# Kernel optimization log

Measured on AMD Instinct MI355X. Metric: run time of the kernel, lower is better.

## Reference

```python
import jax, jax.numpy as jnp
import numpy as np

NPOINT = 2048
NSAMPLE = 32
BN_EPS = 1e-5


def fps(xyz_t, npoint):
    """Furthest point sampling. xyz_t: [B,N,3] -> idx [B,npoint] (starts at index 0)."""
    B, N, _ = xyz_t.shape

    def step(carry, _):
        dist, last = carry  # dist [B,N], last [B]
        centroid = jnp.take_along_axis(xyz_t, last[:, None, None], axis=1)  # [B,1,3]
        d = jnp.sum((xyz_t - centroid) ** 2, axis=-1)  # [B,N]
        dist = jnp.minimum(dist, d)
        nxt = jnp.argmax(dist, axis=1).astype(jnp.int32)
        return (dist, nxt), last

    init = (jnp.full((B, N), 1e10, xyz_t.dtype), jnp.zeros((B,), jnp.int32))
    _, idx = jax.lax.scan(step, init, None, length=npoint)  # [npoint,B]
    return jnp.transpose(idx)  # [B,npoint]


def knn(k, query_t, ref_t):
    """query_t [B,S,3], ref_t [B,N,3] -> k-nearest indices [B,S,k]."""
    d = (jnp.sum(query_t ** 2, -1)[:, :, None]
         + jnp.sum(ref_t ** 2, -1)[:, None, :]
         - 2.0 * jnp.einsum('bsc,bnc->bsn', query_t, ref_t))  # [B,S,N]
    _, idx = jax.lax.top_k(-d, k)
    return idx


def group(feat_t, idx):
    """feat_t [B,N,C], idx [B,S,K] -> [B,S,K,C] gathered neighbors."""
    return jax.vmap(lambda f, i: f[i])(feat_t, idx)


def setup_inputs():
    key = jax.random.key(0)
    ks = jax.random.split(key, 8)
    B, N, C, D = 8, 8192, 3, 3
    mlp = [32, 32, 64]
    inp = {
        'xyz': jax.random.normal(ks[0], (B, C, N), jnp.float32),
        'points': jax.random.normal(ks[1], (B, D, N), jnp.float32),
    }
    last = D + 3  # conv input channels = in_channel + 3
    for i, oc in enumerate(mlp):
        inp[f'w{i}'] = jax.random.normal(ks[2 + i], (oc, last), jnp.float32) * (1.0 / np.sqrt(last))
        inp[f'g{i}'] = jnp.ones((oc,), jnp.float32)
        inp[f'b{i}'] = jnp.zeros((oc,), jnp.float32)
        last = oc
    return inp


def reference(xyz, points, w0, g0, b0, w1, g1, b1, w2, g2, b2):
    xyz_t = jnp.transpose(xyz, (0, 2, 1))        # [B,N,3]
    points_t = jnp.transpose(points, (0, 2, 1))  # [B,N,D]

    fps_idx = fps(xyz_t, NPOINT)                             # [B,S]
    new_xyz_t = jax.vmap(lambda f, i: f[i])(xyz_t, fps_idx)  # [B,S,3]

    knn_idx = knn(NSAMPLE, new_xyz_t, xyz_t)                 # [B,S,K]
    grouped_xyz = group(xyz_t, knn_idx)                      # [B,S,K,3]
    pos_diff = grouped_xyz - new_xyz_t[:, :, None, :]        # [B,S,K,3]
    grouped_pts = group(points_t, knn_idx)                   # [B,S,K,D]

    x = jnp.concatenate([pos_diff, grouped_pts], axis=-1)    # [B,S,K,3+D]
    for w, g, b in ((w0, g0, b0), (w1, g1, b1), (w2, g2, b2)):
        x = jnp.einsum('oc,bskc->bsko', w, x)                # 1x1 conv, no bias
        mean = jnp.mean(x, axis=(0, 1, 2))                   # BatchNorm2d (training stats)
        var = jnp.var(x, axis=(0, 1, 2))
        x = jax.nn.relu(g * (x - mean) * jax.lax.rsqrt(var + BN_EPS) + b)

    new_points = jnp.max(x, axis=2)  # max over K neighbors -> [B,S,C']
    new_xyz = jnp.transpose(new_xyz_t, (0, 2, 1))      # [B,3,S]
    new_points = jnp.transpose(new_points, (0, 2, 1))  # [B,C',S]
    return (new_xyz, new_points, fps_idx)
```

## Files before the change

kernel.cpp:

```cpp
#include <hip/hip_runtime.h>
#include <hip/hip_bf16.h>
#include <math.h>


#define NB 8
#define NN 8192
#define NS 2048
#define NK 32

typedef float f32x2 __attribute__((ext_vector_type(2)));

__device__ __forceinline__ f32x2 pk_mul(f32x2 a, f32x2 b) {
  f32x2 d; asm("v_pk_mul_f32 %0, %1, %2" : "=v"(d) : "v"(a), "v"(b)); return d;
}
__device__ __forceinline__ f32x2 pk_add(f32x2 a, f32x2 b) {
  f32x2 d; asm("v_pk_add_f32 %0, %1, %2" : "=v"(d) : "v"(a), "v"(b)); return d;
}
__device__ __forceinline__ f32x2 pk_sub(f32x2 a, f32x2 b) {
  f32x2 d;
  asm("v_pk_add_f32 %0, %1, %2 neg_lo:[0,1] neg_hi:[0,1]" : "=v"(d) : "v"(a), "v"(b));
  return d;
}

__global__ __launch_bounds__(256) void prep_kernel(const float* __restrict__ xyz,
                                                   const float* __restrict__ pts,
                                                   float4* __restrict__ xyz4,
                                                   float4* __restrict__ pts4) {
  int g = blockIdx.x * 256 + threadIdx.x;
  int b = g >> 13, n = g & 8191;
  const float* xb = xyz + b * 3 * NN;
  float x = xb[n], y = xb[NN + n], z = xb[2 * NN + n];
  xyz4[g] = make_float4(x, y, z, fmaf(x, x, fmaf(y, y, z * z)));
  const float* pb = pts + b * 3 * NN;
  pts4[g] = make_float4(pb[n], pb[NN + n], pb[2 * NN + n], 0.f);
}

template <int CTRL>
__device__ __forceinline__ float dpp_max(float v) {
  int o = __builtin_amdgcn_update_dpp(__float_as_int(v), __float_as_int(v),
                                      CTRL, 0xf, 0xf, false);
  return fmaxf(v, __int_as_float(o));
}

__global__ __launch_bounds__(512, 1) void fps_kernel(const float4* __restrict__ xyz4,
                                                     float* __restrict__ out_nxyz,
                                                     float* __restrict__ out_fps,
                                                     float4* __restrict__ nxyz4) {
#pragma clang fp contract(off)
  int b = blockIdx.x, tid = threadIdx.x;
  int lane = tid & 63, wid = tid >> 6;
  __shared__ float4 tbl[NN];
  __shared__ unsigned long long kslot[2][8];
  const float4* xb = xyz4 + b * NN;

  f32x2 px[8], py[8], pz[8], dist[8];
#pragma unroll
  for (int jj = 0; jj < 8; ++jj) {
    float4 t0 = xb[(tid << 4) + 2 * jj];
    float4 t1 = xb[(tid << 4) + 2 * jj + 1];
    tbl[(tid << 4) + 2 * jj] = t0;
    tbl[(tid << 4) + 2 * jj + 1] = t1;
    px[jj] = (f32x2){t0.x, t1.x};
    py[jj] = (f32x2){t0.y, t1.y};
    pz[jj] = (f32x2){t0.z, t1.z};
    dist[jj] = (f32x2){1e10f, 1e10f};
  }

  float4 c0 = xb[0];
  float cx = c0.x, cy = c0.y, cz = c0.z;
  float* onx = out_nxyz + b * 3 * NS;
  if (tid == 0) {
    nxyz4[b * NS] = c0;
    onx[0] = c0.x;
    onx[NS] = c0.y;
    onx[2 * NS] = c0.z;
    out_fps[b * NS] = 0.f;
  }

  for (int s = 1; s < NS; ++s) {
    f32x2 c2x = {cx, cx}, c2y = {cy, cy}, c2z = {cz, cz};
#pragma unroll
    for (int jj = 0; jj < 8; ++jj) {
      f32x2 dx = pk_sub(px[jj], c2x);
      f32x2 dy = pk_sub(py[jj], c2y);
      f32x2 dz = pk_sub(pz[jj], c2z);
      f32x2 dd = pk_add(pk_add(pk_mul(dx, dx), pk_mul(dy, dy)), pk_mul(dz, dz));
      dist[jj] = __builtin_elementwise_min(dist[jj], dd);
    }
    f32x2 m2 = dist[0];
#pragma unroll
    for (int jj = 1; jj < 8; ++jj) m2 = __builtin_elementwise_max(m2, dist[jj]);
    float best = fmaxf(m2[0], m2[1]);
    int bj = 0;
#pragma unroll
    for (int j = 15; j >= 0; --j)
      bj = (dist[j >> 1][j & 1] == best) ? j : bj;

    float mm = best;
    mm = dpp_max<0x111>(mm);
    mm = dpp_max<0x112>(mm);
    mm = dpp_max<0x114>(mm);
    mm = dpp_max<0x118>(mm);
    mm = dpp_max<0x142>(mm);
    mm = dpp_max<0x143>(mm);
    float wmax = __int_as_float(__builtin_amdgcn_readlane(__float_as_int(mm), 63));

    unsigned long long bl = __ballot(best == wmax);
    int l0 = __ffsll(bl) - 1;
    int gw = __builtin_amdgcn_readlane((tid << 4) + bj, l0);

    if (lane == 0)
      kslot[s & 1][wid] = (((unsigned long long)__float_as_uint(wmax)) << 32) |
                          (unsigned)(8191 - gw);
    __syncthreads();

    const ulonglong2* kv = (const ulonglong2*)kslot[s & 1];
    ulonglong2 q0 = kv[0], q1 = kv[1], q2 = kv[2], q3 = kv[3];
    unsigned long long a0 = q0.x > q0.y ? q0.x : q0.y;
    unsigned long long a1 = q1.x > q1.y ? q1.x : q1.y;
    unsigned long long a2 = q2.x > q2.y ? q2.x : q2.y;
    unsigned long long a3 = q3.x > q3.y ? q3.x : q3.y;
    unsigned long long b0 = a0 > a1 ? a0 : a1;
    unsigned long long b1 = a2 > a3 ? a2 : a3;
    unsigned long long km = b0 > b1 ? b0 : b1;
    int gid = 8191 - (int)((unsigned)km & 0x1FFFu);
    gid = __builtin_amdgcn_readfirstlane(gid);

    float4 c = tbl[gid];
    cx = c.x; cy = c.y; cz = c.z;
    if (tid == 0) {
      nxyz4[b * NS + s] = c;
      onx[s] = c.x;
      onx[NS + s] = c.y;
      onx[2 * NS + s] = c.z;
      out_fps[b * NS + s] = (float)gid;
    }
  }
}

__device__ __forceinline__ void insert32(float (&a)[32], float f) {
#pragma unroll
  for (int i = 31; i >= 1; --i) a[i] = fminf(a[i], fmaxf(a[i - 1], f));
  a[0] = fminf(a[0], f);
}

__global__ __launch_bounds__(256) void knn_kernel(const float4* __restrict__ xyz4,
                                                  const float4* __restrict__ nxyz4,
                                                  int* __restrict__ knn) {
  __shared__ float lbuf[256][33];
  int b = blockIdx.x >> 5, tile = blockIdx.x & 31;
  int tid = threadIdx.x;
  int q = tid & 63, chunk = tid >> 6;
  float4 Q = nxyz4[b * NS + tile * 64 + q];
  float qq = Q.w;
  float mx = -2.f * Q.x, my = -2.f * Q.y, mz = -2.f * Q.z;
  float arr[32];
#pragma unroll
  for (int i = 0; i < 32; ++i) arr[i] = __uint_as_float(0x7f7fffffu);

  const float4* refs = xyz4 + b * NN + chunk * 2048;
  int rbase = chunk * 2048;
  for (int r = 0; r < 2048; ++r) {
    float4 R = refs[r];
    float d = fmaf(R.x, mx, fmaf(R.y, my, fmaf(R.z, mz, R.w + qq)));
    d = fmaxf(d, 0.f);
    float f = __uint_as_float((__float_as_uint(d) & 0xFFFFE000u) | (unsigned)(rbase + r));
    if (f < arr[31]) insert32(arr, f);
  }
#pragma unroll
  for (int i = 0; i < 32; ++i) lbuf[tid][i] = arr[i];
  __syncthreads();
  if (tid < 64) {
    for (int c = 1; c < 4; ++c)
      for (int i = 0; i < 32; ++i) {
        float f = lbuf[c * 64 + tid][i];
        if (f < arr[31]) insert32(arr, f);
      }
    int base = (b * NS + tile * 64 + tid) * NK;
#pragma unroll
    for (int i = 0; i < 32; ++i) knn[base + i] = (int)(__float_as_uint(arr[i]) & 0x1FFFu);
  }
}

template <int STAGE>
__global__ __launch_bounds__(256) void mlp_kernel(
    const float4* __restrict__ xyz4, const float4* __restrict__ pts4,
    const float4* __restrict__ nxyz4, const int* __restrict__ knn,
    const float* __restrict__ w0, const float* __restrict__ w1,
    const float* __restrict__ w2, const float* __restrict__ ab,
    float* __restrict__ partials, float* __restrict__ out_np) {
  constexpr int C = (STAGE == 2) ? 64 : 32;
  constexpr int SM = (STAGE == 3) ? 8 * 64 * 32 : 512;
  __shared__ float smem[SM];
  int blk = blockIdx.x;
  int b = blk >> 6, s0 = (blk & 63) * 32;
  int tid = threadIdx.x, sl = tid & 31, ksec = tid >> 5;
  int lane = tid & 63, wid = tid >> 6;
  int s = s0 + sl;
  float4 Q = nxyz4[b * NS + s];
  const float4* xb = xyz4 + b * NN;
  const float4* pb = pts4 + b * NN;
  const int* kb = knn + (b * NS + s) * NK + ksec * 4;

  float acc1[(STAGE == 3) ? 64 : C];
  float acc2[(STAGE == 3) ? 1 : C];
  if constexpr (STAGE == 3) {
#pragma unroll
    for (int o = 0; o < 64; ++o) acc1[o] = -3.4e38f;
  } else {
#pragma unroll
    for (int o = 0; o < C; ++o) { acc1[o] = 0.f; acc2[o] = 0.f; }
  }

  for (int kk = 0; kk < 4; ++kk) {
    int nid = kb[kk];
    float4 R = xb[nid];
    float4 P = pb[nid];
    float x0[6] = {R.x - Q.x, R.y - Q.y, R.z - Q.z, P.x, P.y, P.z};
    float h[32];
#pragma unroll
    for (int o = 0; o < 32; ++o) {
      float a = w0[o * 6] * x0[0];
#pragma unroll
      for (int c = 1; c < 6; ++c) a = fmaf(w0[o * 6 + c], x0[c], a);
      h[o] = a;
    }
    if constexpr (STAGE == 0) {
#pragma unroll
      for (int o = 0; o < 32; ++o) { acc1[o] += h[o]; acc2[o] = fmaf(h[o], h[o], acc2[o]); }
    } else {
#pragma unroll
      for (int o = 0; o < 32; ++o) h[o] = fmaxf(fmaf(h[o], ab[o], ab[64 + o]), 0.f);
      float h1[32];
#pragma unroll
      for (int o = 0; o < 32; ++o) {
        float a = 0.f;
#pragma unroll
        for (int i = 0; i < 32; ++i) a = fmaf(w1[o * 32 + i], h[i], a);
        h1[o] = a;
      }
      if constexpr (STAGE == 1) {
#pragma unroll
        for (int o = 0; o < 32; ++o) { acc1[o] += h1[o]; acc2[o] = fmaf(h1[o], h1[o], acc2[o]); }
      } else {
#pragma unroll
        for (int o = 0; o < 32; ++o) h1[o] = fmaxf(fmaf(h1[o], ab[128 + o], ab[192 + o]), 0.f);
#pragma unroll
        for (int o = 0; o < 64; ++o) {
          float a = 0.f;
#pragma unroll
          for (int i = 0; i < 32; ++i) a = fmaf(w2[o * 32 + i], h1[i], a);
          if constexpr (STAGE == 2) {
            acc1[o] += a;
            acc2[o] = fmaf(a, a, acc2[o]);
          } else {
            acc1[o] = fmaxf(acc1[o], fmaxf(fmaf(a, ab[256 + o], ab[320 + o]), 0.f));
          }
        }
      }
    }
  }

  if constexpr (STAGE < 3) {
#pragma unroll
    for (int o = 0; o < C; ++o) {
      float v1 = acc1[o], v2 = acc2[o];
#pragma unroll
      for (int d = 1; d < 64; d <<= 1) { v1 += __shfl_xor(v1, d); v2 += __shfl_xor(v2, d); }
      acc1[o] = v1; acc2[o] = v2;
    }
    if (lane == 0) {
#pragma unroll
      for (int o = 0; o < C; ++o) {
        smem[wid * 2 * C + o] = acc1[o];
        smem[wid * 2 * C + C + o] = acc2[o];
      }
    }
    __syncthreads();
    if (tid < 2 * C) {
      float v = smem[tid] + smem[2 * C + tid] + smem[4 * C + tid] + smem[6 * C + tid];
      partials[blk * 128 + tid] = v;
    }
  } else {
#pragma unroll
    for (int o = 0; o < 64; ++o) smem[ksec * 2048 + o * 32 + sl] = acc1[o];
    __syncthreads();
#pragma unroll
    for (int i = 0; i < 8; ++i) {
      int e = i * 256 + tid;
      int ch = e >> 5, ss = e & 31;
      float v = smem[ch * 32 + ss];
#pragma unroll
      for (int ks = 1; ks < 8; ++ks) v = fmaxf(v, smem[ks * 2048 + ch * 32 + ss]);
      out_np[b * 64 * NS + ch * NS + s0 + ss] = v;
    }
  }
}

__global__ __launch_bounds__(256) void finalize_kernel(const float* __restrict__ partials,
                                                       const float* __restrict__ g,
                                                       const float* __restrict__ bt,
                                                       float* __restrict__ ab, int C) {
  __shared__ float sm[256];
  int tid = threadIdx.x;
  int ch = tid & 127, half = tid >> 7;
  float acc = 0.f;
  if (ch < 2 * C) {
    const float* p = partials + half * 256 * 128 + ch;
    for (int i = 0; i < 256; ++i) acc += p[i * 128];
  }
  sm[half * 128 + ch] = acc;
  __syncthreads();
  if (tid < C) {
    float s1 = sm[tid] + sm[128 + tid];
    float s2 = sm[C + tid] + sm[128 + C + tid];
    const float ninv = 1.0f / 524288.0f;
    float mean = s1 * ninv;
    float var = s2 * ninv - mean * mean;
    float inv = 1.0f / sqrtf(var + 1e-5f);
    float a = g[tid] * inv;
    ab[tid] = a;
    ab[64 + tid] = bt[tid] - mean * a;
  }
}

extern "C" void kernel_launch(void* const* d_in, const int* in_sizes, int n_in,
                              void* d_out, int out_size, void* d_ws, size_t ws_size,
                              hipStream_t stream) {
  const float* xyz = (const float*)d_in[0];
  const float* pts = (const float*)d_in[1];
  const float* w0 = (const float*)d_in[2];
  const float* g0 = (const float*)d_in[3];
  const float* b0 = (const float*)d_in[4];
  const float* w1 = (const float*)d_in[5];
  const float* g1 = (const float*)d_in[6];
  const float* b1 = (const float*)d_in[7];
  const float* w2 = (const float*)d_in[8];
  const float* g2 = (const float*)d_in[9];
  const float* b2 = (const float*)d_in[10];
  float* out = (float*)d_out;
  float* ws = (float*)d_ws;

  float4* xyz4 = (float4*)ws;
  float4* pts4 = (float4*)(ws + 262144);
  float4* nxyz4 = (float4*)(ws + 524288);
  int* knn = (int*)(ws + 589824);
  float* partials = ws + 1114112;
  float* ab = ws + 1310720;
  float* out_np = out + 49152;
  float* out_fps = out + 1097728;

  prep_kernel<<<256, 256, 0, stream>>>(xyz, pts, xyz4, pts4);
  fps_kernel<<<NB, 512, 0, stream>>>(xyz4, out, out_fps, nxyz4);
  knn_kernel<<<256, 256, 0, stream>>>(xyz4, nxyz4, knn);

  mlp_kernel<0><<<512, 256, 0, stream>>>(xyz4, pts4, nxyz4, knn, w0, w1, w2, ab, partials, nullptr);
  finalize_kernel<<<1, 256, 0, stream>>>(partials, g0, b0, ab, 32);
  mlp_kernel<1><<<512, 256, 0, stream>>>(xyz4, pts4, nxyz4, knn, w0, w1, w2, ab, partials + 65536, nullptr);
  finalize_kernel<<<1, 256, 0, stream>>>(partials + 65536, g1, b1, ab + 128, 32);
  mlp_kernel<2><<<512, 256, 0, stream>>>(xyz4, pts4, nxyz4, knn, w0, w1, w2, ab, partials + 131072, nullptr);
  finalize_kernel<<<1, 256, 0, stream>>>(partials + 131072, g2, b2, ab + 256, 64);
  mlp_kernel<3><<<512, 256, 0, stream>>>(xyz4, pts4, nxyz4, knn, w0, w1, w2, ab, nullptr, out_np);
}
```

Measured before the change: 3.097 ms.

## Halve FPS block to 256 threads with 32 scalar points per thread

The furthest-point-sampling kernel now runs 4 waves per batch instead of 8, each thread holding 32 points in scalar registers instead of 16 in packed-float pairs. The aim is a cheaper cross-wave reduction and barrier per step, with fewer slots to combine. The per-thread argmax now uses a tree max followed by a bitmask search for the winning index, run only in lanes that hold the wave maximum. In exchange each thread does twice the distance work, using scalar instead of packed arithmetic, and register pressure rises.

```diff
diff --git a/kernel.cpp b/kernel.cpp
--- a/kernel.cpp
+++ b/kernel.cpp
@@ -7,20 +7,6 @@
 #define NN 8192
 #define NS 2048
 #define NK 32
-
-typedef float f32x2 __attribute__((ext_vector_type(2)));
-
-__device__ __forceinline__ f32x2 pk_mul(f32x2 a, f32x2 b) {
-  f32x2 d; asm("v_pk_mul_f32 %0, %1, %2" : "=v"(d) : "v"(a), "v"(b)); return d;
-}
-__device__ __forceinline__ f32x2 pk_add(f32x2 a, f32x2 b) {
-  f32x2 d; asm("v_pk_add_f32 %0, %1, %2" : "=v"(d) : "v"(a), "v"(b)); return d;
-}
-__device__ __forceinline__ f32x2 pk_sub(f32x2 a, f32x2 b) {
-  f32x2 d;
-  asm("v_pk_add_f32 %0, %1, %2 neg_lo:[0,1] neg_hi:[0,1]" : "=v"(d) : "v"(a), "v"(b));
-  return d;
-}
 
 __global__ __launch_bounds__(256) void prep_kernel(const float* __restrict__ xyz,
                                                    const float* __restrict__ pts,
@@ -42,7 +28,7 @@
   return fmaxf(v, __int_as_float(o));
 }
 
-__global__ __launch_bounds__(512, 1) void fps_kernel(const float4* __restrict__ xyz4,
+__global__ __launch_bounds__(256, 1) void fps_kernel(const float4* __restrict__ xyz4,
                                                      float* __restrict__ out_nxyz,
                                                      float* __restrict__ out_fps,
                                                      float4* __restrict__ nxyz4) {
@@ -50,20 +36,16 @@
   int b = blockIdx.x, tid = threadIdx.x;
   int lane = tid & 63, wid = tid >> 6;
   __shared__ float4 tbl[NN];
-  __shared__ unsigned long long kslot[2][8];
+  __shared__ unsigned long long kslot[2][4];
   const float4* xb = xyz4 + b * NN;
 
-  f32x2 px[8], py[8], pz[8], dist[8];
-#pragma unroll
-  for (int jj = 0; jj < 8; ++jj) {
-    float4 t0 = xb[(tid << 4) + 2 * jj];
-    float4 t1 = xb[(tid << 4) + 2 * jj + 1];
-    tbl[(tid << 4) + 2 * jj] = t0;
-    tbl[(tid << 4) + 2 * jj + 1] = t1;
-    px[jj] = (f32x2){t0.x, t1.x};
-    py[jj] = (f32x2){t0.y, t1.y};
-    pz[jj] = (f32x2){t0.z, t1.z};
-    dist[jj] = (f32x2){1e10f, 1e10f};
+  float px[32], py[32], pz[32], dist[32];
+#pragma unroll
+  for (int j = 0; j < 32; ++j) {
+    float4 t = xb[(tid << 5) + j];
+    tbl[(tid << 5) + j] = t;
+    px[j] = t.x; py[j] = t.y; pz[j] = t.z;
+    dist[j] = 1e10f;
   }
 
   float4 c0 = xb[0];
@@ -78,23 +60,24 @@
   }
 
   for (int s = 1; s < NS; ++s) {
-    f32x2 c2x = {cx, cx}, c2y = {cy, cy}, c2z = {cz, cz};
-#pragma unroll
-    for (int jj = 0; jj < 8; ++jj) {
-      f32x2 dx = pk_sub(px[jj], c2x);
-      f32x2 dy = pk_sub(py[jj], c2y);
-      f32x2 dz = pk_sub(pz[jj], c2z);
-      f32x2 dd = pk_add(pk_add(pk_mul(dx, dx), pk_mul(dy, dy)), pk_mul(dz, dz));
-      dist[jj] = __builtin_elementwise_min(dist[jj], dd);
-    }
-    f32x2 m2 = dist[0];
-#pragma unroll
-    for (int jj = 1; jj < 8; ++jj) m2 = __builtin_elementwise_max(m2, dist[jj]);
-    float best = fmaxf(m2[0], m2[1]);
-    int bj = 0;
-#pragma unroll
-    for (int j = 15; j >= 0; --j)
-      bj = (dist[j >> 1][j & 1] == best) ? j : bj;
+#pragma unroll
+    for (int j = 0; j < 32; ++j) {
+      float dx = px[j] - cx;
+      float dy = py[j] - cy;
+      float dz = pz[j] - cz;
+      float d = (dx * dx + dy * dy) + dz * dz;
+      dist[j] = fminf(dist[j], d);
+    }
+    float t16[16];
+#pragma unroll
+    for (int j = 0; j < 16; ++j) t16[j] = fmaxf(dist[j], dist[j + 16]);
+    float t8[8];
+#pragma unroll
+    for (int j = 0; j < 8; ++j) t8[j] = fmaxf(t16[j], t16[j + 8]);
+    float t4[4];
+#pragma unroll
+    for (int j = 0; j < 4; ++j) t4[j] = fmaxf(t8[j], t8[j + 4]);
+    float best = fmaxf(fmaxf(t4[0], t4[2]), fmaxf(t4[1], t4[3]));
 
     float mm = best;
     mm = dpp_max<0x111>(mm);
@@ -107,7 +90,22 @@
 
     unsigned long long bl = __ballot(best == wmax);
     int l0 = __ffsll(bl) - 1;
-    int gw = __builtin_amdgcn_readlane((tid << 4) + bj, l0);
+
+    int bj = 0;
+    if (best == wmax) {
+      unsigned bits[32];
+#pragma unroll
+      for (int j = 0; j < 32; ++j) bits[j] = (dist[j] == best) ? (1u << j) : 0u;
+#pragma unroll
+      for (int j = 0; j < 16; ++j) bits[j] |= bits[j + 16];
+#pragma unroll
+      for (int j = 0; j < 8; ++j) bits[j] |= bits[j + 8];
+#pragma unroll
+      for (int j = 0; j < 4; ++j) bits[j] |= bits[j + 4];
+      unsigned mask = (bits[0] | bits[2]) | (bits[1] | bits[3]);
+      bj = __ffs(mask) - 1;
+    }
+    int gw = __builtin_amdgcn_readlane((tid << 5) + bj, l0);
 
     if (lane == 0)
       kslot[s & 1][wid] = (((unsigned long long)__float_as_uint(wmax)) << 32) |
@@ -115,14 +113,10 @@
     __syncthreads();
 
     const ulonglong2* kv = (const ulonglong2*)kslot[s & 1];
-    ulonglong2 q0 = kv[0], q1 = kv[1], q2 = kv[2], q3 = kv[3];
+    ulonglong2 q0 = kv[0], q1 = kv[1];
     unsigned long long a0 = q0.x > q0.y ? q0.x : q0.y;
     unsigned long long a1 = q1.x > q1.y ? q1.x : q1.y;
-    unsigned long long a2 = q2.x > q2.y ? q2.x : q2.y;
-    unsigned long long a3 = q3.x > q3.y ? q3.x : q3.y;
-    unsigned long long b0 = a0 > a1 ? a0 : a1;
-    unsigned long long b1 = a2 > a3 ? a2 : a3;
-    unsigned long long km = b0 > b1 ? b0 : b1;
+    unsigned long long km = a0 > a1 ? a0 : a1;
     int gid = 8191 - (int)((unsigned)km & 0x1FFFu);
     gid = __builtin_amdgcn_readfirstlane(gid);
 
@@ -351,7 +345,7 @@
   float* out_fps = out + 1097728;
 
   prep_kernel<<<256, 256, 0, stream>>>(xyz, pts, xyz4, pts4);
-  fps_kernel<<<NB, 512, 0, stream>>>(xyz4, out, out_fps, nxyz4);
+  fps_kernel<<<NB, 256, 0, stream>>>(xyz4, out, out_fps, nxyz4);
   knn_kernel<<<256, 256, 0, stream>>>(xyz4, nxyz4, knn);
 
   mlp_kernel<0><<<512, 256, 0, stream>>>(xyz4, pts4, nxyz4, knn, w0, w1, w2, ab, partials, nullptr);
```

Measured after the change: 3.846 ms. 24.2% more time.
